# Optimization experiments

Measured on AMD Instinct MI355X. Metric: run time of the kernel, lower is better.

The kernel has to match this reference:

```python
import jax, jax.numpy as jnp
import numpy as np

TRANSFORM = "exp"  # matches init kwarg transform='exp'


def setup_inputs() -> dict:
    key = jax.random.key(0)
    k1, k2 = jax.random.split(key)
    scores = jax.random.normal(k1, (64, 1024, 1), dtype=jnp.float32)
    labels = jax.random.normal(k2, (64, 1024), dtype=jnp.float32)
    return {"scores": scores, "labels": labels}


def _transform(x):
    if TRANSFORM == "exp":
        return jnp.exp(x)
    if TRANSFORM == "sigmoid":
        return jax.nn.sigmoid(x)
    return x


def reference(scores, labels):
    # scores: (B, N, 1), labels: (B, N)
    B, N, _ = scores.shape
    s = scores[..., 0]
    if N % 2 != 0:
        s = s[:, :-1]
        labels = labels[:, :-1]
        N -= 1
    h = N // 2
    # sort labels descending -> ground-truth permutation; gather scores
    order = jnp.argsort(-labels, axis=1)              # (B, N)
    osc = jnp.take_along_axis(s, order, axis=1)        # (B, N) ordered scores

    # Pairwise f(os[u] - os[v]); original loops are
    #   denom(j) = sum_{u=j..h} sum_{v=h+j-1..N-1, v!=u} f(os[u]-os[v])
    F = _transform(osc[:, :, None] - osc[:, None, :])  # (B, N, N)
    # suffix sums over v: C[b,u,s] = sum_{v>=s} F[b,u,v]
    C = jnp.flip(jnp.cumsum(jnp.flip(F, -1), axis=-1), -1)
    j = jnp.arange(h)
    A = C[:, :, h + j - 1]                             # (B, N, h): v-range sums
    u = jnp.arange(N)
    umask = ((u[:, None] >= j[None, :]) & (u[:, None] <= h)).astype(osc.dtype)  # (N, h)
    denom = jnp.einsum('bnj,nj->bj', A, umask)         # (B, h)
    # remove diagonal u==v terms: overlap count is max(0, 2-j), each worth f(0)
    f0 = 1.0 if TRANSFORM == 'exp' else (0.5 if TRANSFORM == 'sigmoid' else 0.0)
    denom = denom - f0 * jnp.maximum(0, 2 - j).astype(osc.dtype)
    # numer(j) = f(os[j] - os[N-1-j])
    numer = _transform(osc[:, :h] - osc[:, ::-1][:, :h])  # (B, h)
    loss = -jnp.sum(jnp.log(numer / denom)) / B
    return loss
```

## Files before the change

### kernel.cpp

```cpp
#include <hip/hip_runtime.h>
#include <math.h>

#define NN 1024
#define HH 512
#define BB 64
#define NT 1024
#define MAGIC 0x5A5A5A5Au

__global__ __launch_bounds__(NT) void lfl_fused(const float* __restrict__ scores,
                                                const float* __restrict__ labels,
                                                float* __restrict__ out,
                                                unsigned long long* __restrict__ slots) {
    __shared__ float2 kv[2][NN];
    __shared__ float osc_l[NN];
    __shared__ float sa_l[NN];
    __shared__ float sb_l[NN];
    __shared__ float wA[16], wB[16];

    const int b    = blockIdx.x;
    const int t    = threadIdx.x;
    const int lane = t & 63;
    const int wv   = t >> 6;

    float k = -labels[b * NN + t];
    float v = scores[b * NN + t];

    auto shfl_ce = [&](int stride, bool up) {
        float kp = __shfl_xor(k, stride);
        float vp = __shfl_xor(v, stride);
        bool lower = ((t & stride) == 0);
        bool take  = (up == lower) ? (kp < k) : (kp > k);
        if (take) { k = kp; v = vp; }
    };

    int pb = 0;
    auto lds_ex = [&](int stride, bool up) {
        kv[pb][t] = make_float2(k, v);
        __syncthreads();
        float2 p = kv[pb][t ^ stride];
        bool lower = ((t & stride) == 0);
        bool take  = (up == lower) ? (p.x < k) : (p.x > k);
        if (take) { k = p.x; v = p.y; }
        pb ^= 1;
    };

    #pragma unroll
    for (int size = 2; size <= 64; size <<= 1) {
        bool up = ((t & size) == 0);
        #pragma unroll
        for (int s = size >> 1; s >= 1; s >>= 1) shfl_ce(s, up);
    }
    #pragma unroll
    for (int size = 128; size <= 1024; size <<= 1) {
        bool up = ((t & size) == 0);
        for (int s = size >> 1; s >= 64; s >>= 1) lds_ex(s, up);
        #pragma unroll
        for (int s = 32; s >= 1; s >>= 1) shfl_ce(s, up);
    }

    float Sa = __expf(v);
    float Sb = __expf(-v);
    #pragma unroll
    for (int d = 1; d < 64; d <<= 1) {
        float xa = __shfl_down(Sa, d);
        float xb = __shfl_down(Sb, d);
        if (lane + d < 64) { Sa += xa; Sb += xb; }
    }
    if (lane == 0) { wA[wv] = Sa; wB[wv] = Sb; }
    __syncthreads();
    float addA = 0.f, addB = 0.f;
    for (int w = wv + 1; w < 16; ++w) { addA += wA[w]; addB += wB[w]; }
    float sa = Sa + addA;
    float sb = Sb + addB;

    osc_l[t] = v;
    sa_l[t]  = sa;
    sb_l[t]  = sb;
    __syncthreads();

    float acc = 0.f;
    if (t < HH) {
        float P = sa - sa_l[513];
        float T = sb_l[511 + t];
        float denom = P * T - (t == 0 ? 2.0f : (t == 1 ? 1.0f : 0.0f));
        acc = (v - osc_l[NN - 1 - t]) - __logf(denom);
    }

    #pragma unroll
    for (int off = 32; off > 0; off >>= 1) acc += __shfl_down(acc, off);
    if (lane == 0) wA[wv] = acc;
    __syncthreads();

    float part = 0.f;
    if (t == 0) {
        #pragma unroll
        for (int w = 0; w < 16; ++w) part += wA[w];
        if (b != 0) {
            unsigned lo = __float_as_uint(part);
            unsigned long long pk = ((unsigned long long)(lo ^ MAGIC) << 32) | (unsigned long long)lo;
            atomicExch(&slots[b], pk);
        }
    }

    if (b == 0 && t < 64) {
        float x = (t == 0) ? part : 0.f;
        if (t > 0) {
            unsigned long long pk;
            do {
                pk = atomicAdd(&slots[t], 0ULL);
            } while ((unsigned)(pk >> 32) != ((unsigned)pk ^ MAGIC));
            x = __uint_as_float((unsigned)pk);
        }
        #pragma unroll
        for (int off = 32; off > 0; off >>= 1) x += __shfl_down(x, off);
        if (t == 0) out[0] = -x / (float)BB;
    }
}

extern "C" void kernel_launch(void* const* d_in, const int* in_sizes, int n_in,
                              void* d_out, int out_size, void* d_ws, size_t ws_size,
                              hipStream_t stream) {
    const float* scores = (const float*)d_in[0];
    const float* labels = (const float*)d_in[1];
    float* out = (float*)d_out;
    unsigned long long* slots = (unsigned long long*)d_ws;

    lfl_fused<<<BB, NT, 0, stream>>>(scores, labels, out, slots);
}
```

Before: 14.22 us.

## Sort two elements per thread with 512-thread blocks in bitonic sort

The block size is halved so each thread holds two consecutive elements. The first bitonic stage becomes an in-register compare-exchange, and every other stage exchanges float4 pairs through shuffles or LDS. This cuts the thread count and the number of barrier-synchronised LDS stages, and it loads inputs as float2. In exchange each thread does more work per step, and the suffix-sum and final-loss indexing is rebuilt around element pairs.

Result: slower. 14.78 us (+3.9%).

```diff
diff --git a/kernel.cpp b/kernel.cpp
--- a/kernel.cpp
+++ b/kernel.cpp
@@ -4,62 +4,93 @@
 #define NN 1024
 #define HH 512
 #define BB 64
-#define NT 1024
+#define NT 512
 #define MAGIC 0x5A5A5A5Au
 
 __global__ __launch_bounds__(NT) void lfl_fused(const float* __restrict__ scores,
                                                 const float* __restrict__ labels,
                                                 float* __restrict__ out,
                                                 unsigned long long* __restrict__ slots) {
-    __shared__ float2 kv[2][NN];
+    __shared__ float4 kv[2][NT];
     __shared__ float osc_l[NN];
     __shared__ float sa_l[NN];
     __shared__ float sb_l[NN];
-    __shared__ float wA[16], wB[16];
+    __shared__ float wA[8], wB[8];
 
     const int b    = blockIdx.x;
     const int t    = threadIdx.x;
     const int lane = t & 63;
     const int wv   = t >> 6;
 
-    float k = -labels[b * NN + t];
-    float v = scores[b * NN + t];
+    const float2 lb2 = *reinterpret_cast<const float2*>(&labels[b * NN + 2 * t]);
+    const float2 sc2 = *reinterpret_cast<const float2*>(&scores[b * NN + 2 * t]);
+    float k0 = -lb2.x, k1 = -lb2.y;
+    float v0 = sc2.x,  v1 = sc2.y;
 
-    auto shfl_ce = [&](int stride, bool up) {
-        float kp = __shfl_xor(k, stride);
-        float vp = __shfl_xor(v, stride);
-        bool lower = ((t & stride) == 0);
-        bool take  = (up == lower) ? (kp < k) : (kp > k);
-        if (take) { k = kp; v = vp; }
+    auto ce_intra = [&](bool up) {
+        bool sw = up ? (k0 > k1) : (k0 < k1);
+        if (sw) { float tk = k0; k0 = k1; k1 = tk; float tv = v0; v0 = v1; v1 = tv; }
     };
-
+    auto ce_shfl = [&](int ts, bool up) {
+        bool lower = ((t & ts) == 0);
+        bool cond  = (up == lower);
+        float kp0 = __shfl_xor(k0, ts), vp0 = __shfl_xor(v0, ts);
+        float kp1 = __shfl_xor(k1, ts), vp1 = __shfl_xor(v1, ts);
+        bool g0 = cond ? (kp0 < k0) : (kp0 > k0);
+        bool g1 = cond ? (kp1 < k1) : (kp1 > k1);
+        if (g0) { k0 = kp0; v0 = vp0; }
+        if (g1) { k1 = kp1; v1 = vp1; }
+    };
     int pb = 0;
-    auto lds_ex = [&](int stride, bool up) {
-        kv[pb][t] = make_float2(k, v);
+    auto ce_lds = [&](int ts, bool up) {
+        kv[pb][t] = make_float4(k0, v0, k1, v1);
         __syncthreads();
-        float2 p = kv[pb][t ^ stride];
-        bool lower = ((t & stride) == 0);
-        bool take  = (up == lower) ? (p.x < k) : (p.x > k);
-        if (take) { k = p.x; v = p.y; }
+        float4 q = kv[pb][t ^ ts];
+        bool lower = ((t & ts) == 0);
+        bool cond  = (up == lower);
+        bool g0 = cond ? (q.x < k0) : (q.x > k0);
+        bool g1 = cond ? (q.z < k1) : (q.z > k1);
+        if (g0) { k0 = q.x; v0 = q.y; }
+        if (g1) { k1 = q.z; v1 = q.w; }
         pb ^= 1;
     };
 
+    ce_intra((t & 1) == 0);
     #pragma unroll
-    for (int size = 2; size <= 64; size <<= 1) {
-        bool up = ((t & size) == 0);
+    for (int S = 4; S <= 128; S <<= 1) {
+        bool up = ((t & (S >> 1)) == 0);
         #pragma unroll
-        for (int s = size >> 1; s >= 1; s >>= 1) shfl_ce(s, up);
+        for (int ts = S >> 2; ts >= 1; ts >>= 1) ce_shfl(ts, up);
+        ce_intra(up);
     }
-    #pragma unroll
-    for (int size = 128; size <= 1024; size <<= 1) {
-        bool up = ((t & size) == 0);
-        for (int s = size >> 1; s >= 64; s >>= 1) lds_ex(s, up);
+    {
+        bool up = ((t & 128) == 0);
+        ce_lds(64, up);
         #pragma unroll
-        for (int s = 32; s >= 1; s >>= 1) shfl_ce(s, up);
+        for (int ts = 32; ts >= 1; ts >>= 1) ce_shfl(ts, up);
+        ce_intra(up);
+    }
+    {
+        bool up = ((t & 256) == 0);
+        ce_lds(128, up);
+        ce_lds(64, up);
+        #pragma unroll
+        for (int ts = 32; ts >= 1; ts >>= 1) ce_shfl(ts, up);
+        ce_intra(up);
+    }
+    {
+        ce_lds(256, true);
+        ce_lds(128, true);
+        ce_lds(64, true);
+        #pragma unroll
+        for (int ts = 32; ts >= 1; ts >>= 1) ce_shfl(ts, true);
+        ce_intra(true);
     }
 
-    float Sa = __expf(v);
-    float Sb = __expf(-v);
+    float a0 = __expf(v0),  a1 = __expf(v1);
+    float e0 = __expf(-v0), e1 = __expf(-v1);
+    float Ta = a0 + a1, Tb = e0 + e1;
+    float Sa = Ta, Sb = Tb;
     #pragma unroll
     for (int d = 1; d < 64; d <<= 1) {
         float xa = __shfl_down(Sa, d);
@@ -69,22 +100,22 @@
     if (lane == 0) { wA[wv] = Sa; wB[wv] = Sb; }
     __syncthreads();
     float addA = 0.f, addB = 0.f;
-    for (int w = wv + 1; w < 16; ++w) { addA += wA[w]; addB += wB[w]; }
-    float sa = Sa + addA;
-    float sb = Sb + addB;
+    for (int w = wv + 1; w < 8; ++w) { addA += wA[w]; addB += wB[w]; }
+    float saE0 = Sa + addA;
+    float sbE0 = Sb + addB;
 
-    osc_l[t] = v;
-    sa_l[t]  = sa;
-    sb_l[t]  = sb;
+    osc_l[2 * t]     = v0;
+    osc_l[2 * t + 1] = v1;
+    sa_l[2 * t]      = saE0;
+    sa_l[2 * t + 1]  = saE0 - a0;
+    sb_l[2 * t]      = sbE0;
+    sb_l[2 * t + 1]  = sbE0 - e0;
     __syncthreads();
 
-    float acc = 0.f;
-    if (t < HH) {
-        float P = sa - sa_l[513];
-        float T = sb_l[511 + t];
-        float denom = P * T - (t == 0 ? 2.0f : (t == 1 ? 1.0f : 0.0f));
-        acc = (v - osc_l[NN - 1 - t]) - __logf(denom);
-    }
+    float P = sa_l[t] - sa_l[513];
+    float T = sb_l[511 + t];
+    float denom = P * T - (t == 0 ? 2.0f : (t == 1 ? 1.0f : 0.0f));
+    float acc = (osc_l[t] - osc_l[NN - 1 - t]) - __logf(denom);
 
     #pragma unroll
     for (int off = 32; off > 0; off >>= 1) acc += __shfl_down(acc, off);
@@ -94,7 +125,7 @@
     float part = 0.f;
     if (t == 0) {
         #pragma unroll
-        for (int w = 0; w < 16; ++w) part += wA[w];
+        for (int w = 0; w < 8; ++w) part += wA[w];
         if (b != 0) {
             unsigned lo = __float_as_uint(part);
             unsigned long long pk = ((unsigned long long)(lo ^ MAGIC) << 32) | (unsigned long long)lo;
```
